# Optimization experiments

Measured on AMD Instinct MI355X. Metric: run time of the kernel, lower is better.

The kernel has to match this reference:

```python
import jax, jax.numpy as jnp
import numpy as np

N = 100000      # nodes
E = 1600000     # edges (avg in-degree 16)
IN_DIM = 256
HID_DIM = 256
OUT_DIM = 32
K = 16          # propagation hops


def _xavier(key, fan_in, fan_out, gain=1.0):
    a = gain * (6.0 / (fan_in + fan_out)) ** 0.5
    return jax.random.uniform(key, (fan_in, fan_out), jnp.float32, -a, a)


def setup_inputs() -> dict:
    key = jax.random.key(0)
    ks = jax.random.split(key, 8)
    feats = jax.random.normal(ks[0], (N, IN_DIM), jnp.float32)
    relu_gain = 2.0 ** 0.5
    W1 = _xavier(ks[1], IN_DIM, HID_DIM, relu_gain)
    b1 = jnp.zeros((HID_DIM,), jnp.float32)
    W2 = _xavier(ks[2], HID_DIM, HID_DIM, relu_gain)
    b2 = jnp.zeros((HID_DIM,), jnp.float32)
    W3 = _xavier(ks[3], HID_DIM, OUT_DIM, 1.0)
    b3 = jnp.zeros((OUT_DIM,), jnp.float32)
    s = _xavier(ks[4], OUT_DIM, 1, 1.0)  # sigmoid gain = 1.0
    src = jax.random.randint(ks[5], (E,), 0, N, jnp.int32)
    dst = jax.random.randint(ks[6], (E,), 0, N, jnp.int32)
    return {"feats": feats, "W1": W1, "b1": b1, "W2": W2, "b2": b2,
            "W3": W3, "b3": b3, "s": s, "src": src, "dst": dst}


def reference(feats, W1, b1, W2, b2, W3, b3, s, src, dst):
    # MLP stack (dropout is identity at inference)
    x = jax.nn.relu(feats @ W1 + b1)
    x = jax.nn.relu(x @ W2 + b2)
    x = x @ W3 + b3  # [N, OUT_DIM]

    # symmetric degree normalization from in-degrees (count of dst)
    degs = jax.ops.segment_sum(jnp.ones((E,), jnp.float32), dst, num_segments=N)
    norm = jnp.where(degs > 0, degs ** -0.5, 0.0)[:, None]  # [N,1]

    # k-hop normalized SpMM propagation: h <- D^-1/2 A^T D^-1/2 h
    def step(h, _):
        msgs = (h * norm)[src]                                  # gather, [E,D]
        h2 = jax.ops.segment_sum(msgs, dst, num_segments=N) * norm
        return h2, h2

    _, hs = jax.lax.scan(step, x, None, length=K)  # [K, N, D]
    H = jnp.concatenate([x[None], hs], axis=0).transpose(1, 0, 2)  # [N, K+1, D]

    # sigmoid-gated attention pooling over hops
    S = jax.nn.sigmoid(jnp.einsum('nkd,d->nk', H, s[:, 0]))  # [N, K+1]
    out = jnp.einsum('nk,nkd->nd', S, H)                      # [N, D]
    return out
```

## Files before the change

kernel.cpp:

```cpp
#include <hip/hip_runtime.h>
#include <hip/hip_bf16.h>
#include <cstdint>

typedef short bf16x8 __attribute__((ext_vector_type(8)));
typedef float f32x4 __attribute__((ext_vector_type(4)));
typedef unsigned short u16x8 __attribute__((ext_vector_type(8)));

#define BSHIFT 8
#define NBMAX 512

__device__ __forceinline__ ushort f2bf(float x) {
  uint32_t u = __float_as_uint(x);
  u += 0x7FFFu + ((u >> 16) & 1u);
  return (ushort)(u >> 16);
}
__device__ __forceinline__ float bf2f(ushort b) {
  return __uint_as_float((uint32_t)b << 16);
}

__device__ __forceinline__ void gload16(const void* g, void* l) {
  __builtin_amdgcn_global_load_lds((const __attribute__((address_space(1))) uint32_t*)g,
                                   (__attribute__((address_space(3))) uint32_t*)l, 16, 0, 0);
}

__global__ __launch_bounds__(256) void k_f32_to_bf16(const float* __restrict__ in,
                                                     ushort* __restrict__ out, int n4) {
  int i = blockIdx.x * 256 + threadIdx.x;
  if (i >= n4) return;
  const float4 v = reinterpret_cast<const float4*>(in)[i];
  ushort4 o;
  o.x = f2bf(v.x); o.y = f2bf(v.y); o.z = f2bf(v.z); o.w = f2bf(v.w);
  reinterpret_cast<ushort4*>(out)[i] = o;
}

__global__ __launch_bounds__(256) void k_convT(const float* __restrict__ W,
                                               ushort* __restrict__ Bt, int K, int Nc) {
  int i = blockIdx.x * 256 + threadIdx.x;
  if (i >= K * Nc) return;
  int nn = i / K, kk = i - nn * K;
  Bt[i] = f2bf(W[kk * Nc + nn]);
}

__global__ __launch_bounds__(256) void k_gemm1(const ushort* __restrict__ A,
                                               const ushort* __restrict__ Bt,
                                               const float* __restrict__ bias,
                                               ushort* __restrict__ Cout, int M, int ldc) {
  constexpr int BM = 128, BK = 64, KTOT = 256;
  constexpr int WM = 64, WN = 64, MR = 4, NR = 4;
  __shared__ ushort lA[BM * BK];
  __shared__ ushort lB[BM * BK];
  const int tid = threadIdx.x;
  const int w = tid >> 6, lane = tid & 63;
  const int wr = w >> 1, wc = w & 1;
  const int bm = blockIdx.x * BM;
  const int bn = blockIdx.y * BM;
  f32x4 acc[MR][NR] = {};

  for (int ks = 0; ks < KTOT; ks += BK) {
    #pragma unroll
    for (int c0 = 0; c0 < 4; ++c0) {
      int c = c0 * 256 + tid;
      int r = c >> 3, ch = c & 7;
      int sch = (ch ^ (r & 7)) << 3;
      gload16(A + (size_t)(bm + r) * KTOT + ks + sch, lA + c * 8);
      gload16(Bt + (size_t)(bn + r) * KTOT + ks + sch, lB + c * 8);
    }
    __syncthreads();
    #pragma unroll
    for (int kk = 0; kk < 2; ++kk) {
      bf16x8 af[MR], bfr[NR];
      int kc = kk * 4 + (lane >> 4);
      #pragma unroll
      for (int m = 0; m < MR; ++m) {
        int r = wr * WM + m * 16 + (lane & 15);
        af[m] = *reinterpret_cast<const bf16x8*>(lA + r * BK + (kc ^ (r & 7)) * 8);
      }
      #pragma unroll
      for (int n = 0; n < NR; ++n) {
        int r = wc * WN + n * 16 + (lane & 15);
        bfr[n] = *reinterpret_cast<const bf16x8*>(lB + r * BK + (kc ^ (r & 7)) * 8);
      }
      #pragma unroll
      for (int m = 0; m < MR; ++m)
        #pragma unroll
        for (int n = 0; n < NR; ++n)
          acc[m][n] = __builtin_amdgcn_mfma_f32_16x16x32_bf16(af[m], bfr[n], acc[m][n], 0, 0, 0);
    }
    __syncthreads();
  }
  #pragma unroll
  for (int m = 0; m < MR; ++m) {
    #pragma unroll
    for (int n = 0; n < NR; ++n) {
      int col = bn + wc * WN + n * 16 + (lane & 15);
      float bv = bias[col];
      #pragma unroll
      for (int j = 0; j < 4; ++j) {
        int row = bm + wr * WM + m * 16 + (lane >> 4) * 4 + j;
        if (row < M) {
          float v = fmaxf(acc[m][n][j] + bv, 0.f);
          Cout[(size_t)row * ldc + col] = f2bf(v);
        }
      }
    }
  }
}

__global__ __launch_bounds__(256) void k_gemm23(const ushort* __restrict__ x1,
                                                const ushort* __restrict__ w2t,
                                                const float* __restrict__ b2,
                                                const ushort* __restrict__ w3t,
                                                const float* __restrict__ b3,
                                                const float* __restrict__ svec,
                                                const float* __restrict__ nrm,
                                                float* __restrict__ xout,
                                                ushort* __restrict__ hs0, int M) {
  constexpr int BM = 64, BK = 64, KTOT = 256;
  constexpr int MR = 4, NR = 4;
  __shared__ char smem[40960];
  ushort* lA = (ushort*)smem;
  ushort* lB = (ushort*)(smem + 8192);
  ushort* lh2 = (ushort*)smem;
  const int tid = threadIdx.x;
  const int wv = tid >> 6, lane = tid & 63;
  const int bm = blockIdx.x * BM;
  f32x4 acc[MR][NR] = {};

  for (int ks = 0; ks < KTOT; ks += BK) {
    #pragma unroll
    for (int c0 = 0; c0 < 2; ++c0) {
      int c = c0 * 256 + tid;
      int r = c >> 3, ch = c & 7;
      gload16(x1 + (size_t)(bm + r) * KTOT + ks + ((ch ^ (r & 7)) << 3), lA + c * 8);
    }
    #pragma unroll
    for (int c0 = 0; c0 < 8; ++c0) {
      int c = c0 * 256 + tid;
      int r = c >> 3, ch = c & 7;
      gload16(w2t + (size_t)r * KTOT + ks + ((ch ^ (r & 7)) << 3), lB + c * 8);
    }
    __syncthreads();
    #pragma unroll
    for (int kk = 0; kk < 2; ++kk) {
      bf16x8 af[MR], bfr[NR];
      int kc = kk * 4 + (lane >> 4);
      #pragma unroll
      for (int m = 0; m < MR; ++m) {
        int r = m * 16 + (lane & 15);
        af[m] = *reinterpret_cast<const bf16x8*>(lA + r * BK + (kc ^ (r & 7)) * 8);
      }
      #pragma unroll
      for (int n = 0; n < NR; ++n) {
        int r = wv * 64 + n * 16 + (lane & 15);
        bfr[n] = *reinterpret_cast<const bf16x8*>(lB + r * BK + (kc ^ (r & 7)) * 8);
      }
      #pragma unroll
      for (int m = 0; m < MR; ++m)
        #pragma unroll
        for (int n = 0; n < NR; ++n)
          acc[m][n] = __builtin_amdgcn_mfma_f32_16x16x32_bf16(af[m], bfr[n], acc[m][n], 0, 0, 0);
    }
    __syncthreads();
  }

  #pragma unroll
  for (int n = 0; n < NR; ++n) {
    int col = wv * 64 + n * 16 + (lane & 15);
    float bv = b2[col];
    #pragma unroll
    for (int m = 0; m < MR; ++m) {
      #pragma unroll
      for (int j = 0; j < 4; ++j) {
        int row = m * 16 + (lane >> 4) * 4 + j;
        float v = fmaxf(acc[m][n][j] + bv, 0.f);
        int ch = col >> 3;
        int within = col & 7;
        lh2[row * 256 + ((ch ^ (row & 7)) << 3) + within] = f2bf(v);
      }
    }
  }
  __syncthreads();

  f32x4 acc3[2] = {};
  #pragma unroll
  for (int ks3 = 0; ks3 < 8; ++ks3) {
    int row = wv * 16 + (lane & 15);
    int kc = ks3 * 4 + (lane >> 4);
    bf16x8 af = *reinterpret_cast<const bf16x8*>(lh2 + row * 256 + ((kc ^ (row & 7)) << 3));
    #pragma unroll
    for (int n = 0; n < 2; ++n) {
      int col = n * 16 + (lane & 15);
      bf16x8 bfr = *reinterpret_cast<const bf16x8*>(w3t + (size_t)col * KTOT + kc * 8);
      acc3[n] = __builtin_amdgcn_mfma_f32_16x16x32_bf16(af, bfr, acc3[n], 0, 0, 0);
    }
  }
  float bb0 = b3[(lane & 15)];
  float bb1 = b3[16 + (lane & 15)];
  float sv0 = svec[(lane & 15)];
  float sv1 = svec[16 + (lane & 15)];
  #pragma unroll
  for (int j = 0; j < 4; ++j) {
    float x0 = acc3[0][j] + bb0;
    float x1v = acc3[1][j] + bb1;
    float p = x0 * sv0 + x1v * sv1;
    #pragma unroll
    for (int msk = 1; msk <= 8; msk <<= 1) p += __shfl_xor(p, msk);
    float g = 1.f / (1.f + __expf(-p));
    int row = bm + wv * 16 + (lane >> 4) * 4 + j;
    if (row < M) {
      float nv = nrm[row];
      xout[(size_t)row * 32 + (lane & 15)] = g * x0;
      xout[(size_t)row * 32 + 16 + (lane & 15)] = g * x1v;
      hs0[(size_t)row * 32 + (lane & 15)] = f2bf(x0 * nv);
      hs0[(size_t)row * 32 + 16 + (lane & 15)] = f2bf(x1v * nv);
    }
  }
}

__global__ __launch_bounds__(256) void k_bucket_hist(const int* __restrict__ dst,
                                                     int* __restrict__ bhist, int E) {
  __shared__ int lh[NBMAX];
  const int t = threadIdx.x;
  const int base = blockIdx.x * 4096;
  for (int i = t; i < NBMAX; i += 256) lh[i] = 0;
  __syncthreads();
  #pragma unroll
  for (int j = 0; j < 16; ++j) {
    int e = base + t + j * 256;
    if (e < E) atomicAdd(&lh[dst[e] >> BSHIFT], 1);
  }
  __syncthreads();
  for (int i = t; i < NBMAX; i += 256)
    if (lh[i]) atomicAdd(&bhist[i], lh[i]);
}

__global__ __launch_bounds__(256) void k_bucket_scan(const int* __restrict__ bhist,
                                                     int* __restrict__ bbase) {
  __shared__ int sh[256];
  int t = threadIdx.x;
  int v0 = bhist[2 * t], v1 = bhist[2 * t + 1];
  int s = v0 + v1;
  sh[t] = s;
  __syncthreads();
  for (int off = 1; off < 256; off <<= 1) {
    int x = (t >= off) ? sh[t - off] : 0;
    __syncthreads();
    sh[t] += x;
    __syncthreads();
  }
  int pre = sh[t] - s;
  bbase[2 * t] = pre;
  bbase[2 * t + 1] = pre + v0;
  if (t == 255) bbase[NBMAX] = sh[255];
}

__global__ __launch_bounds__(256) void k_bucket_scatter(const int* __restrict__ src,
                                                        const int* __restrict__ dst,
                                                        const int* __restrict__ bbase,
                                                        int* __restrict__ gfill,
                                                        int* __restrict__ tmp,
                                                        int E, int nbuck) {
  __shared__ int lhist[NBMAX];
  __shared__ int lbase[NBMAX];
  const int t = threadIdx.x;
  const int base = blockIdx.x * 4096;
  for (int i = t; i < NBMAX; i += 256) lhist[i] = 0;
  __syncthreads();
  int myd[16];
  #pragma unroll
  for (int j = 0; j < 16; ++j) {
    int e = base + t + j * 256;
    myd[j] = (e < E) ? dst[e] : -1;
    if (myd[j] >= 0) atomicAdd(&lhist[myd[j] >> BSHIFT], 1);
  }
  __syncthreads();
  for (int i = t; i < nbuck; i += 256) {
    int c = lhist[i];
    lbase[i] = (c > 0) ? atomicAdd(&gfill[i], c) : 0;
    lhist[i] = 0;
  }
  __syncthreads();
  #pragma unroll
  for (int j = 0; j < 16; ++j) {
    int e = base + t + j * 256;
    if (myd[j] >= 0) {
      int b = myd[j] >> BSHIFT;
      int r = atomicAdd(&lhist[b], 1);
      int pos = bbase[b] + lbase[b] + r;
      tmp[pos] = src[e] | ((myd[j] & 255) << 17);
    }
  }
}

__global__ __launch_bounds__(256) void k_bucket_sort(const int* __restrict__ tmp,
                                                     const int* __restrict__ bbase,
                                                     int* __restrict__ rp,
                                                     float* __restrict__ nrm,
                                                     float* __restrict__ invdeg,
                                                     float* __restrict__ sdeg,
                                                     int* __restrict__ ss,
                                                     int Nn, int E) {
  __shared__ int lcnt[256];
  __shared__ int sh[256];
  __shared__ int lpre[256];
  __shared__ int lfill[256];
  const int t = threadIdx.x;
  const int b = blockIdx.x;
  const int node0 = b << BSHIFT;
  const int seg0 = bbase[b], seg1 = bbase[b + 1];
  lcnt[t] = 0;
  lfill[t] = 0;
  __syncthreads();
  for (int i = seg0 + t; i < seg1; i += 256)
    atomicAdd(&lcnt[tmp[i] >> 17], 1);
  __syncthreads();
  int c = lcnt[t];
  sh[t] = c;
  __syncthreads();
  for (int off = 1; off < 256; off <<= 1) {
    int x = (t >= off) ? sh[t - off] : 0;
    __syncthreads();
    sh[t] += x;
    __syncthreads();
  }
  int pre = seg0 + sh[t] - c;
  lpre[t] = pre;
  int node = node0 + t;
  if (node < Nn) {
    rp[node] = pre;
    nrm[node] = (c > 0) ? rsqrtf((float)c) : 0.f;
    invdeg[node] = (c > 0) ? (1.f / (float)c) : 0.f;
    sdeg[node] = sqrtf((float)c);
  }
  if (b == 0 && t == 0) rp[Nn] = E;
  __syncthreads();
  for (int i = seg0 + t; i < seg1; i += 256) {
    int p = tmp[i];
    int n = p >> 17;
    int r = atomicAdd(&lfill[n], 1);
    ss[lpre[n] + r] = p & 0x1FFFF;
  }
}

__global__ __launch_bounds__(256) void k_prop(const ushort* __restrict__ hs_in,
                                              ushort* __restrict__ hs_out,
                                              const int* __restrict__ rp,
                                              const int* __restrict__ ss,
                                              const float* __restrict__ invdeg, int Nn) {
  const int wave = threadIdx.x >> 6;
  const int lane = threadIdx.x & 63;
  const int e16 = lane >> 2;
  const int d4 = lane & 3;
  const int v = blockIdx.x * 4 + wave;
  if (v >= Nn) return;
  const int beg = rp[v], end = rp[v + 1];
  float a0 = 0, a1 = 0, a2 = 0, a3 = 0, a4 = 0, a5 = 0, a6 = 0, a7 = 0;
  for (int i = beg + e16; i < end; i += 16) {
    int u = ss[i];
    u16x8 h = *reinterpret_cast<const u16x8*>(hs_in + (size_t)u * 32 + d4 * 8);
    a0 += bf2f(h[0]); a1 += bf2f(h[1]); a2 += bf2f(h[2]); a3 += bf2f(h[3]);
    a4 += bf2f(h[4]); a5 += bf2f(h[5]); a6 += bf2f(h[6]); a7 += bf2f(h[7]);
  }
  #pragma unroll
  for (int m = 4; m <= 32; m <<= 1) {
    a0 += __shfl_xor(a0, m); a1 += __shfl_xor(a1, m);
    a2 += __shfl_xor(a2, m); a3 += __shfl_xor(a3, m);
    a4 += __shfl_xor(a4, m); a5 += __shfl_xor(a5, m);
    a6 += __shfl_xor(a6, m); a7 += __shfl_xor(a7, m);
  }
  if (e16 == 0) {
    const float idv = invdeg[v];
    u16x8 hn;
    hn[0] = f2bf(a0 * idv); hn[1] = f2bf(a1 * idv); hn[2] = f2bf(a2 * idv); hn[3] = f2bf(a3 * idv);
    hn[4] = f2bf(a4 * idv); hn[5] = f2bf(a5 * idv); hn[6] = f2bf(a6 * idv); hn[7] = f2bf(a7 * idv);
    *reinterpret_cast<u16x8*>(hs_out + (size_t)v * 32 + d4 * 8) = hn;
  }
}

__global__ __launch_bounds__(256) void k_pool(const ushort* __restrict__ hsF,
                                              const ushort* __restrict__ hsX,
                                              const ushort* __restrict__ hs16,
                                              const float* __restrict__ sdeg,
                                              const float* __restrict__ svec,
                                              float* __restrict__ xout, int Nn) {
  const int t = blockIdx.x * 256 + threadIdx.x;
  const int v = t >> 2;
  const int d4 = t & 3;
  if (v >= Nn) return;
  const float sd = sdeg[v];
  const float4 svA = *reinterpret_cast<const float4*>(svec + d4 * 8);
  const float4 svB = *reinterpret_cast<const float4*>(svec + d4 * 8 + 4);
  const size_t seg = (size_t)Nn * 32;
  const size_t off = (size_t)v * 32 + d4 * 8;
  float o0 = 0, o1 = 0, o2 = 0, o3 = 0, o4 = 0, o5 = 0, o6 = 0, o7 = 0;
  #pragma unroll
  for (int k = 1; k <= 16; ++k) {
    const ushort* hp = (k < 8) ? (hsF + (size_t)k * seg)
                     : (k < 16) ? (hsX + (size_t)(k - 8) * seg)
                                : hs16;
    u16x8 h = *reinterpret_cast<const u16x8*>(hp + off);
    float h0 = bf2f(h[0]) * sd, h1 = bf2f(h[1]) * sd, h2 = bf2f(h[2]) * sd, h3 = bf2f(h[3]) * sd;
    float h4 = bf2f(h[4]) * sd, h5 = bf2f(h[5]) * sd, h6 = bf2f(h[6]) * sd, h7 = bf2f(h[7]) * sd;
    float p = h0 * svA.x + h1 * svA.y + h2 * svA.z + h3 * svA.w
            + h4 * svB.x + h5 * svB.y + h6 * svB.z + h7 * svB.w;
    p += __shfl_xor(p, 1);
    p += __shfl_xor(p, 2);
    const float g = 1.f / (1.f + __expf(-p));
    o0 += g * h0; o1 += g * h1; o2 += g * h2; o3 += g * h3;
    o4 += g * h4; o5 += g * h5; o6 += g * h6; o7 += g * h7;
  }
  float4* oa = reinterpret_cast<float4*>(xout + off);
  float4 q0 = oa[0], q1 = oa[1];
  q0.x += o0; q0.y += o1; q0.z += o2; q0.w += o3;
  q1.x += o4; q1.y += o5; q1.z += o6; q1.w += o7;
  oa[0] = q0; oa[1] = q1;
}

extern "C" void kernel_launch(void* const* d_in, const int* in_sizes, int n_in,
                              void* d_out, int out_size, void* d_ws, size_t ws_size,
                              hipStream_t stream) {
  const float* feats = (const float*)d_in[0];
  const float* W1 = (const float*)d_in[1];
  const float* b1 = (const float*)d_in[2];
  const float* W2 = (const float*)d_in[3];
  const float* b2 = (const float*)d_in[4];
  const float* W3 = (const float*)d_in[5];
  const float* b3 = (const float*)d_in[6];
  const float* svec = (const float*)d_in[7];
  const int* src = (const int*)d_in[8];
  const int* dst = (const int*)d_in[9];

  const int DIN = 256, DH = 256, DOUT = 32, KHOP = 16;
  const int N = in_sizes[0] / DIN;
  const int E = in_sizes[8];
  const int nbuck = (N + (1 << BSHIFT) - 1) >> BSHIFT;

  char* w = (char*)d_ws;
  auto alloc = [&](size_t bytes) {
    char* p = w;
    w += (bytes + 255) & ~(size_t)255;
    return p;
  };
  ushort* featsb = (ushort*)alloc((size_t)N * DIN * 2);
  ushort* x1b = (ushort*)alloc((size_t)N * DH * 2);
  ushort* w1t = (ushort*)alloc((size_t)DIN * DH * 2);
  ushort* w2t = (ushort*)alloc((size_t)DH * DH * 2);
  ushort* w3t = (ushort*)alloc((size_t)DH * DOUT * 2);
  ushort* hs16 = (ushort*)alloc((size_t)N * DOUT * 2);
  float* nrm = (float*)alloc((size_t)N * 4);
  float* invdeg = (float*)alloc((size_t)N * 4);
  float* sdeg = (float*)alloc((size_t)N * 4);
  int* rp  = (int*)alloc((size_t)(N + 1) * 4);
  int* bhist = (int*)alloc((size_t)NBMAX * 4);
  int* bbase = (int*)alloc((size_t)(NBMAX + 1) * 4);
  int* gfill = (int*)alloc((size_t)NBMAX * 4);
  int* ss  = (int*)alloc((size_t)E * 4);
  int* tmp = (int*)alloc((size_t)E * 4);
  float* xout = (float*)d_out;

  const size_t seg = (size_t)N * DOUT;
  auto hsptr = [&](int k) -> ushort* {
    if (k < 8) return featsb + (size_t)k * seg;
    if (k < 16) return x1b + (size_t)(k - 8) * seg;
    return hs16;
  };

  k_f32_to_bf16<<<dim3((N * DIN / 4 + 255) / 256), 256, 0, stream>>>(feats, featsb, N * DIN / 4);
  k_convT<<<dim3((DIN * DH + 255) / 256), 256, 0, stream>>>(W1, w1t, DIN, DH);
  k_convT<<<dim3((DH * DH + 255) / 256), 256, 0, stream>>>(W2, w2t, DH, DH);
  k_convT<<<dim3((DH * DOUT + 255) / 256), 256, 0, stream>>>(W3, w3t, DH, DOUT);

  (void)hipMemsetAsync(bhist, 0, (size_t)NBMAX * 4, stream);
  (void)hipMemsetAsync(gfill, 0, (size_t)NBMAX * 4, stream);
  int nchunk = (E + 4095) / 4096;
  k_bucket_hist<<<dim3(nchunk), 256, 0, stream>>>(dst, bhist, E);
  k_bucket_scan<<<dim3(1), 256, 0, stream>>>(bhist, bbase);
  k_bucket_scatter<<<dim3(nchunk), 256, 0, stream>>>(src, dst, bbase, gfill, tmp, E, nbuck);
  k_bucket_sort<<<dim3(nbuck), 256, 0, stream>>>(tmp, bbase, rp, nrm, invdeg, sdeg, ss, N, E);

  dim3 g1((N + 127) / 128, DH / 128);
  k_gemm1<<<g1, 256, 0, stream>>>(featsb, w1t, b1, x1b, N, DH);
  k_gemm23<<<dim3((N + 63) / 64), 256, 0, stream>>>(x1b, w2t, b2, w3t, b3, svec, nrm, xout,
                                                    hsptr(0), N);

  for (int h = 0; h < KHOP; ++h) {
    k_prop<<<dim3((N + 3) / 4), 256, 0, stream>>>(hsptr(h), hsptr(h + 1), rp, ss, invdeg, N);
  }
  k_pool<<<dim3((N * 4 + 255) / 256), 256, 0, stream>>>(hsptr(0), hsptr(8), hs16, sdeg, svec,
                                                        xout, N);
}
```

Measured before the change: 784.1 us.

## Double-buffer GEMM LDS tiles and issue two edge gathers up front in propagation

```diff
diff --git a/kernel.cpp b/kernel.cpp
--- a/kernel.cpp
+++ b/kernel.cpp
@@ -47,8 +47,8 @@
                                                ushort* __restrict__ Cout, int M, int ldc) {
   constexpr int BM = 128, BK = 64, KTOT = 256;
   constexpr int WM = 64, WN = 64, MR = 4, NR = 4;
-  __shared__ ushort lA[BM * BK];
-  __shared__ ushort lB[BM * BK];
+  __shared__ ushort lA[2][BM * BK];
+  __shared__ ushort lB[2][BM * BK];
   const int tid = threadIdx.x;
   const int w = tid >> 6, lane = tid & 63;
   const int wr = w >> 1, wc = w & 1;
@@ -56,16 +56,22 @@
   const int bn = blockIdx.y * BM;
   f32x4 acc[MR][NR] = {};
 
-  for (int ks = 0; ks < KTOT; ks += BK) {
+  auto stage = [&](int buf, int ks) {
     #pragma unroll
     for (int c0 = 0; c0 < 4; ++c0) {
       int c = c0 * 256 + tid;
       int r = c >> 3, ch = c & 7;
       int sch = (ch ^ (r & 7)) << 3;
-      gload16(A + (size_t)(bm + r) * KTOT + ks + sch, lA + c * 8);
-      gload16(Bt + (size_t)(bn + r) * KTOT + ks + sch, lB + c * 8);
-    }
-    __syncthreads();
+      gload16(A + (size_t)(bm + r) * KTOT + ks + sch, lA[buf] + c * 8);
+      gload16(Bt + (size_t)(bn + r) * KTOT + ks + sch, lB[buf] + c * 8);
+    }
+  };
+
+  stage(0, 0);
+  __syncthreads();
+  int cur = 0;
+  for (int kst = 0; kst < 4; ++kst) {
+    if (kst < 3) stage(cur ^ 1, (kst + 1) * BK);
     #pragma unroll
     for (int kk = 0; kk < 2; ++kk) {
       bf16x8 af[MR], bfr[NR];
@@ -73,12 +79,12 @@
       #pragma unroll
       for (int m = 0; m < MR; ++m) {
         int r = wr * WM + m * 16 + (lane & 15);
-        af[m] = *reinterpret_cast<const bf16x8*>(lA + r * BK + (kc ^ (r & 7)) * 8);
+        af[m] = *reinterpret_cast<const bf16x8*>(lA[cur] + r * BK + (kc ^ (r & 7)) * 8);
       }
       #pragma unroll
       for (int n = 0; n < NR; ++n) {
         int r = wc * WN + n * 16 + (lane & 15);
-        bfr[n] = *reinterpret_cast<const bf16x8*>(lB + r * BK + (kc ^ (r & 7)) * 8);
+        bfr[n] = *reinterpret_cast<const bf16x8*>(lB[cur] + r * BK + (kc ^ (r & 7)) * 8);
       }
       #pragma unroll
       for (int m = 0; m < MR; ++m)
@@ -87,6 +93,7 @@
           acc[m][n] = __builtin_amdgcn_mfma_f32_16x16x32_bf16(af[m], bfr[n], acc[m][n], 0, 0, 0);
     }
     __syncthreads();
+    cur ^= 1;
   }
   #pragma unroll
   for (int m = 0; m < MR; ++m) {
@@ -355,11 +362,30 @@
   if (v >= Nn) return;
   const int beg = rp[v], end = rp[v + 1];
   float a0 = 0, a1 = 0, a2 = 0, a3 = 0, a4 = 0, a5 = 0, a6 = 0, a7 = 0;
-  for (int i = beg + e16; i < end; i += 16) {
-    int u = ss[i];
-    u16x8 h = *reinterpret_cast<const u16x8*>(hs_in + (size_t)u * 32 + d4 * 8);
-    a0 += bf2f(h[0]); a1 += bf2f(h[1]); a2 += bf2f(h[2]); a3 += bf2f(h[3]);
-    a4 += bf2f(h[4]); a5 += bf2f(h[5]); a6 += bf2f(h[6]); a7 += bf2f(h[7]);
+  if (beg < end) {
+    const int i0 = beg + e16;
+    const int i1 = i0 + 16;
+    const int last = end - 1;
+    const int u0 = ss[min(i0, last)];
+    const int u1 = ss[min(i1, last)];
+    const u16x8 h0 = *reinterpret_cast<const u16x8*>(hs_in + (size_t)u0 * 32 + d4 * 8);
+    const u16x8 h1 = *reinterpret_cast<const u16x8*>(hs_in + (size_t)u1 * 32 + d4 * 8);
+    const float m0 = (i0 < end) ? 1.f : 0.f;
+    const float m1 = (i1 < end) ? 1.f : 0.f;
+    a0 = fmaf(m0, bf2f(h0[0]), m1 * bf2f(h1[0]));
+    a1 = fmaf(m0, bf2f(h0[1]), m1 * bf2f(h1[1]));
+    a2 = fmaf(m0, bf2f(h0[2]), m1 * bf2f(h1[2]));
+    a3 = fmaf(m0, bf2f(h0[3]), m1 * bf2f(h1[3]));
+    a4 = fmaf(m0, bf2f(h0[4]), m1 * bf2f(h1[4]));
+    a5 = fmaf(m0, bf2f(h0[5]), m1 * bf2f(h1[5]));
+    a6 = fmaf(m0, bf2f(h0[6]), m1 * bf2f(h1[6]));
+    a7 = fmaf(m0, bf2f(h0[7]), m1 * bf2f(h1[7]));
+    for (int i = i1 + 16; i < end; i += 16) {
+      int u = ss[i];
+      u16x8 h = *reinterpret_cast<const u16x8*>(hs_in + (size_t)u * 32 + d4 * 8);
+      a0 += bf2f(h[0]); a1 += bf2f(h[1]); a2 += bf2f(h[2]); a3 += bf2f(h[3]);
+      a4 += bf2f(h[4]); a5 += bf2f(h[5]); a6 += bf2f(h[6]); a7 += bf2f(h[7]);
+    }
   }
   #pragma unroll
   for (int m = 4; m <= 32; m <<= 1) {
```

New measurement: 776.2 us. About the same (-1.0%).
